# Optimization experiments

Hardware: AMD Instinct MI355X
Metric: run time of the kernel (lower is better)

Reference implementation:

```python
import jax, jax.numpy as jnp
import numpy as np

N, E, IN_DIM, H, HEADS, L, NCLS, NTYPES, NGRAPH = 50000, 800000, 128, 128, 4, 3, 10, 8, 64
C = H // HEADS

def setup_inputs() -> dict:
    key = jax.random.key(0)
    ks = jax.random.split(key, 24)
    inp = {
        'x': jax.random.normal(ks[0], (N, IN_DIM), jnp.float32),
        'edge_index': jax.random.randint(ks[1], (2, E), 0, N, jnp.int64),
        'node_types': jax.random.randint(ks[2], (N,), 0, NTYPES, jnp.int64),
        'batch': jnp.sort(jax.random.randint(ks[3], (N,), 0, NGRAPH, jnp.int64)),
        'W_node': jax.random.normal(ks[4], (IN_DIM, H), jnp.float32) / np.sqrt(IN_DIM),
        'b_node': jnp.zeros((H,), jnp.float32),
        'type_emb': jax.random.normal(ks[5], (NTYPES, H), jnp.float32) * 0.02,
        'W_gat': jax.random.normal(ks[6], (L, H, H), jnp.float32) / np.sqrt(H),
        'a_src': jax.random.normal(ks[7], (L, HEADS, C), jnp.float32) / np.sqrt(C),
        'a_dst': jax.random.normal(ks[8], (L, HEADS, C), jnp.float32) / np.sqrt(C),
        'b_gat': jnp.zeros((L, H), jnp.float32),
        'ln_g': jnp.ones((L, H), jnp.float32),
        'ln_b': jnp.zeros((L, H), jnp.float32),
        'W1': jax.random.normal(ks[9], (H, 2 * H), jnp.float32) / np.sqrt(H),
        'b1': jnp.zeros((2 * H,), jnp.float32),
        'W2': jax.random.normal(ks[10], (2 * H, H), jnp.float32) / np.sqrt(2 * H),
        'b2': jnp.zeros((H,), jnp.float32),
        'W3': jax.random.normal(ks[11], (H, NCLS), jnp.float32) / np.sqrt(H),
        'b3': jnp.zeros((NCLS,), jnp.float32),
    }
    return inp


def _gat_layer(h, src, dst, W, asrc, adst, b):
    # h: [N,H] -> xh: [N,heads,C]
    xh = (h @ W).reshape(N, HEADS, C)
    s_src = jnp.sum(xh * asrc, axis=-1)  # [N,heads]
    s_dst = jnp.sum(xh * adst, axis=-1)
    e = jax.nn.leaky_relu(s_src[src] + s_dst[dst], 0.2)  # [E',heads]
    m = jax.ops.segment_max(e, dst, num_segments=N)      # segment softmax over dst
    ee = jnp.exp(e - m[dst])
    z = jax.ops.segment_sum(ee, dst, num_segments=N)
    alpha = ee / (z[dst] + 1e-16)
    msg = xh[src] * alpha[:, :, None]                    # [E',heads,C]
    out = jax.ops.segment_sum(msg, dst, num_segments=N)
    return out.reshape(N, H) + b


def _layernorm(x, g, b, eps=1e-5):
    mu = jnp.mean(x, -1, keepdims=True)
    var = jnp.mean((x - mu) ** 2, -1, keepdims=True)
    return (x - mu) * jax.lax.rsqrt(var + eps) * g + b


def reference(x, edge_index, node_types, batch, W_node, b_node, type_emb,
              W_gat, a_src, a_dst, b_gat, ln_g, ln_b, W1, b1, W2, b2, W3, b3):
    # PyG GATConv adds self-loops by default
    loops = jnp.arange(N, dtype=edge_index.dtype)
    src = jnp.concatenate([edge_index[0], loops])
    dst = jnp.concatenate([edge_index[1], loops])

    h = x @ W_node + b_node + type_emb[node_types]
    for l in range(L):
        h_prev = h
        h = _gat_layer(h, src, dst, W_gat[l], a_src[l], a_dst[l], b_gat[l])
        h = _layernorm(h, ln_g[l], ln_b[l])
        h = jax.nn.relu(h + h_prev)

    # global_mean_pool over batch (the global-attention h_graph is dead code: overwritten)
    sums = jax.ops.segment_sum(h, batch, num_segments=NGRAPH)
    cnt = jax.ops.segment_sum(jnp.ones((N,), h.dtype), batch, num_segments=NGRAPH)
    hg = sums / jnp.maximum(cnt, 1.0)[:, None]

    z = jax.nn.relu(hg @ W1 + b1)
    z = jax.nn.relu(z @ W2 + b2)
    return z @ W3 + b3
```

## Files before the change

### kernel.cpp

```cpp
#include <hip/hip_runtime.h>
#include <hip/hip_bf16.h>

#define NN 50000
#define EE 800000
#define IN_DIM 128
#define HH 128
#define HEADS 4
#define CC 32
#define LL 3
#define NCLS 10
#define NGRAPH 64
#define SNB ((NN + 1023) / 1024)

using short8 = __attribute__((ext_vector_type(8))) short;
using f32x4 = __attribute__((ext_vector_type(4))) float;

__device__ inline float lrelu(float x) { return fmaxf(x, 0.2f * x); }
__device__ inline float fexp(float x) { return __expf(x); }

__device__ inline float bf2f(ushort u) {
    union { uint32_t i; float f; } c;
    c.i = ((uint32_t)u) << 16;
    return c.f;
}
__device__ inline ushort f2bf(float f) {
    union { float f; uint32_t i; } c;
    c.f = f;
    uint32_t x = c.i;
    uint32_t r = (x + 0x7fffu + ((x >> 16) & 1u)) >> 16;
    return (ushort)r;
}

__device__ inline float wred_sum(float v) {
#pragma unroll
    for (int m = 32; m >= 1; m >>= 1) v += __shfl_xor(v, m, 64);
    return v;
}

__device__ inline float pick4(int h, float a, float b, float c, float d) {
    float ab = (h & 1) ? b : a;
    float cd = (h & 1) ? d : c;
    return (h & 2) ? cd : ab;
}

__global__ __launch_bounds__(256) void convert_x(const float* __restrict__ x,
                                                 ushort* __restrict__ xb) {
    int u = blockIdx.x * 256 + threadIdx.x;
    const float4* x4 = (const float4*)x;
    float4 f0 = x4[u * 2];
    float4 f1 = x4[u * 2 + 1];
    short8 o;
    o[0] = (short)f2bf(f0.x); o[1] = (short)f2bf(f0.y);
    o[2] = (short)f2bf(f0.z); o[3] = (short)f2bf(f0.w);
    o[4] = (short)f2bf(f1.x); o[5] = (short)f2bf(f1.y);
    o[6] = (short)f2bf(f1.z); o[7] = (short)f2bf(f1.w);
    ((short8*)xb)[u] = o;
}

__global__ __launch_bounds__(256) void prep_weights(const float* __restrict__ W_node,
                                                    const float* __restrict__ W_gat,
                                                    ushort* __restrict__ WT) {
    int b = blockIdx.x;
    const float* W = (b == 0) ? W_node : (W_gat + (size_t)(b - 1) * 16384);
    ushort* D = WT + (size_t)b * 16384;
    int t = threadIdx.x;
    int n = t >> 1;
    int k0 = (t & 1) * 64;
    for (int kk = 0; kk < 64; kk++) {
        int k = k0 + kk;
        float v = W[k * 128 + n];
        int u = (k >> 3) ^ (n & 7);
        D[n * 128 + u * 8 + (k & 7)] = f2bf(v);
    }
}

template <int MODE>
__global__ __launch_bounds__(256) void gemm_mfma(
    const ushort* __restrict__ Abf, const ushort* __restrict__ WT,
    ushort* __restrict__ out_bf,
    const float* __restrict__ bias, const int* __restrict__ ntypes,
    const float* __restrict__ temb, int nrows) {
    __shared__ ushort wlds[16384];
    int tid = threadIdx.x;
    int lane = tid & 63;
    int wid = tid >> 6;

    {
        const short8* src = (const short8*)WT;
        short8* dst = (short8*)wlds;
#pragma unroll
        for (int i = 0; i < 8; i++) dst[i * 256 + tid] = src[i * 256 + tid];
    }

    int rbase = blockIdx.x * 64 + wid * 16;
    int arow = rbase + (lane & 15);
    if (arow >= nrows) arow = nrows - 1;
    const short8* arow_p = (const short8*)(Abf + (size_t)arow * 128);
    short8 afr[4];
#pragma unroll
    for (int ks = 0; ks < 4; ks++) afr[ks] = arow_p[ks * 4 + (lane >> 4)];

    __syncthreads();

    f32x4 acc[8];
#pragma unroll
    for (int i = 0; i < 8; i++) acc[i] = (f32x4){0.f, 0.f, 0.f, 0.f};

    int cgrp = lane & 15;
    int kgrp = lane >> 4;
#pragma unroll
    for (int ks = 0; ks < 4; ks++) {
        short8 a = afr[ks];
#pragma unroll
        for (int nt = 0; nt < 8; nt++) {
            int n = nt * 16 + cgrp;
            int u = (ks * 4 + kgrp) ^ (n & 7);
            short8 b = *(const short8*)&wlds[n * 128 + u * 8];
            acc[nt] = __builtin_amdgcn_mfma_f32_16x16x32_bf16(a, b, acc[nt], 0, 0, 0);
        }
    }

    int nts[4];
    if (MODE == 1) {
#pragma unroll
        for (int r = 0; r < 4; r++) {
            int row = rbase + kgrp * 4 + r;
            nts[r] = (row < nrows) ? ntypes[row] : 0;
        }
    }
#pragma unroll
    for (int nt = 0; nt < 8; nt++) {
        int colc = nt * 16 + cgrp;
#pragma unroll
        for (int r = 0; r < 4; r++) {
            int row = rbase + kgrp * 4 + r;
            if (row < nrows) {
                float v = acc[nt][r];
                if (MODE == 1) v += bias[colc] + temb[nts[r] * 128 + colc];
                out_bf[(size_t)row * 128 + colc] = f2bf(v);
            }
        }
    }
}

__global__ __launch_bounds__(256) void attn_scores(
    const ushort* __restrict__ xh, const float* __restrict__ asrc,
    const float* __restrict__ adst, float* __restrict__ s_src,
    float* __restrict__ s_dst, int n) {
    int tid = threadIdx.x;
    int node = blockIdx.x * 16 + (tid >> 4);
    int g = tid & 15;
    if (node >= n) return;
    short8 xv = *(const short8*)(xh + (size_t)node * 128 + g * 8);
    const float4* as4 = (const float4*)(asrc + g * 8);
    const float4* ad4 = (const float4*)(adst + g * 8);
    float4 a0 = as4[0], a1 = as4[1];
    float4 d0 = ad4[0], d1 = ad4[1];
    float xf[8];
#pragma unroll
    for (int k = 0; k < 8; k++) xf[k] = bf2f((ushort)xv[k]);
    float ps = xf[0] * a0.x + xf[1] * a0.y + xf[2] * a0.z + xf[3] * a0.w +
               xf[4] * a1.x + xf[5] * a1.y + xf[6] * a1.z + xf[7] * a1.w;
    float pd = xf[0] * d0.x + xf[1] * d0.y + xf[2] * d0.z + xf[3] * d0.w +
               xf[4] * d1.x + xf[5] * d1.y + xf[6] * d1.z + xf[7] * d1.w;
    ps += __shfl_xor(ps, 1, 64); ps += __shfl_xor(ps, 2, 64);
    pd += __shfl_xor(pd, 1, 64); pd += __shfl_xor(pd, 2, 64);
    if ((g & 3) == 0) {
        s_src[node * 4 + (g >> 2)] = ps;
        s_dst[node * 4 + (g >> 2)] = pd;
    }
}

__global__ void count_slot(const int* __restrict__ dst, int* __restrict__ deg,
                           int* __restrict__ slot, int ne) {
    int i = blockIdx.x * blockDim.x + threadIdx.x;
    if (i < ne) slot[i] = atomicAdd(&deg[dst[i]], 1);
}

__global__ __launch_bounds__(1024) void scan_local(const int* __restrict__ cnt,
                                                   int* __restrict__ rp,
                                                   int* __restrict__ btot, int n) {
    __shared__ int lds[1024];
    int t = threadIdx.x;
    int i = blockIdx.x * 1024 + t;
    int v = (i < n) ? cnt[i] : 0;
    lds[t] = v;
    __syncthreads();
    for (int off = 1; off < 1024; off <<= 1) {
        int u = (t >= off) ? lds[t - off] : 0;
        __syncthreads();
        lds[t] += u;
        __syncthreads();
    }
    if (i < n) rp[i] = lds[t] - v;
    if (t == 1023) btot[blockIdx.x] = lds[1023];
}

__global__ __launch_bounds__(64) void scan_btot(int* __restrict__ btot) {
    int t = threadIdx.x;
    int v = (t < SNB) ? btot[t] : 0;
#pragma unroll
    for (int off = 1; off < 64; off <<= 1) {
        int u = __shfl_up(v, off, 64);
        if (t >= off) v += u;
    }
    if (t < SNB) btot[t] = v;
}

__global__ __launch_bounds__(1024) void scan_add(int* __restrict__ rp,
                                                 const int* __restrict__ btot, int n) {
    int b = blockIdx.x;
    int i = b * 1024 + threadIdx.x;
    int add = (b == 0) ? 0 : btot[b - 1];
    if (i < n) rp[i] += add;
    if (i == 0) rp[n] = EE;
}

__global__ void fill_pass(const int* __restrict__ ei, const int* __restrict__ row_ptr,
                          const int* __restrict__ slot, int* __restrict__ col, int ne) {
    int i = blockIdx.x * blockDim.x + threadIdx.x;
    if (i < ne) {
        int d = ei[ne + i];
        col[row_ptr[d] + slot[i]] = ei[i];
    }
}

__global__ __launch_bounds__(256) void gat_aggregate(
    const ushort* __restrict__ xh, const float* __restrict__ ssrc,
    const float* __restrict__ sdst, const int* __restrict__ row_ptr,
    const int* __restrict__ col, const float* __restrict__ bg,
    const float* __restrict__ lng, const float* __restrict__ lnb,
    ushort* __restrict__ h, int n) {
    int wid = threadIdx.x >> 6;
    int lane = threadIdx.x & 63;
    int node = blockIdx.x * 4 + wid;
    if (node >= n) return;

    int base = row_ptr[node];
    int deg = row_ptr[node + 1] - base;

    float4 sd = ((const float4*)sdst)[node];
    float4 ssf = ((const float4*)ssrc)[node];

    int eg = lane >> 4;
    int g = lane & 15;
    int head = g >> 2;
    float sdH = pick4(head, sd.x, sd.y, sd.z, sd.w);
    float esH = lrelu(pick4(head, ssf.x, ssf.y, ssf.z, ssf.w) + sdH);

    float acc[8];
#pragma unroll
    for (int k = 0; k < 8; k++) acc[k] = 0.f;
    float z = 0.f;

    if (eg == 0) {
        float w = fexp(esH);
        z = w;
        short8 xv = *(const short8*)(xh + (size_t)node * 128 + g * 8);
#pragma unroll
        for (int k = 0; k < 8; k++) acc[k] += w * bf2f((ushort)xv[k]);
    }

    int nit = (deg + 3) >> 2;
#pragma unroll 2
    for (int t = 0; t < nit; t++) {
        int j = t * 4 + eg;
        if (j < deg) {
            int s = col[base + j];
            float4 ss = ((const float4*)ssrc)[s];
            float sH = pick4(head, ss.x, ss.y, ss.z, ss.w);
            float w = fexp(lrelu(sH + sdH));
            z += w;
            short8 xv = *(const short8*)(xh + (size_t)s * 128 + g * 8);
#pragma unroll
            for (int k = 0; k < 8; k++) acc[k] += w * bf2f((ushort)xv[k]);
        }
    }
#pragma unroll
    for (int k = 0; k < 8; k++) {
        acc[k] += __shfl_xor(acc[k], 16, 64);
        acc[k] += __shfl_xor(acc[k], 32, 64);
    }
    z += __shfl_xor(z, 16, 64);
    z += __shfl_xor(z, 32, 64);
    float iz = 1.f / (z + 1e-16f);

    const float4* bg4 = (const float4*)(bg + g * 8);
    float4 b0 = bg4[0], b1 = bg4[1];
    float o[8];
    o[0] = acc[0] * iz + b0.x; o[1] = acc[1] * iz + b0.y;
    o[2] = acc[2] * iz + b0.z; o[3] = acc[3] * iz + b0.w;
    o[4] = acc[4] * iz + b1.x; o[5] = acc[5] * iz + b1.y;
    o[6] = acc[6] * iz + b1.z; o[7] = acc[7] * iz + b1.w;

    float ls = 0.f;
#pragma unroll
    for (int k = 0; k < 8; k++) ls += o[k];
    float mu = wred_sum(ls) * (1.f / 512.f);
    float vs = 0.f;
#pragma unroll
    for (int k = 0; k < 8; k++) {
        o[k] -= mu;
        vs += o[k] * o[k];
    }
    float var = wred_sum(vs) * (1.f / 512.f);
    float rs = rsqrtf(var + 1e-5f);

    if (eg == 0) {
        const float4* lg4 = (const float4*)(lng + g * 8);
        const float4* lb4 = (const float4*)(lnb + g * 8);
        float4 g0 = lg4[0], g1 = lg4[1];
        float4 q0 = lb4[0], q1 = lb4[1];
        ushort* hr = h + (size_t)node * 128 + g * 8;
        short8 prev = *(const short8*)hr;
        float y[8];
        y[0] = fmaxf(o[0] * rs * g0.x + q0.x + bf2f((ushort)prev[0]), 0.f);
        y[1] = fmaxf(o[1] * rs * g0.y + q0.y + bf2f((ushort)prev[1]), 0.f);
        y[2] = fmaxf(o[2] * rs * g0.z + q0.z + bf2f((ushort)prev[2]), 0.f);
        y[3] = fmaxf(o[3] * rs * g0.w + q0.w + bf2f((ushort)prev[3]), 0.f);
        y[4] = fmaxf(o[4] * rs * g1.x + q1.x + bf2f((ushort)prev[4]), 0.f);
        y[5] = fmaxf(o[5] * rs * g1.y + q1.y + bf2f((ushort)prev[5]), 0.f);
        y[6] = fmaxf(o[6] * rs * g1.z + q1.z + bf2f((ushort)prev[6]), 0.f);
        y[7] = fmaxf(o[7] * rs * g1.w + q1.w + bf2f((ushort)prev[7]), 0.f);
        short8 ob;
#pragma unroll
        for (int k = 0; k < 8; k++) ob[k] = (short)f2bf(y[k]);
        *(short8*)hr = ob;
    }
}

__global__ __launch_bounds__(256) void pool_kernel(const ushort* __restrict__ h,
                                                   const int* __restrict__ batch,
                                                   float* __restrict__ sums,
                                                   int* __restrict__ cnts, int n) {
    int c = threadIdx.x & 127;
    int half = threadIdx.x >> 7;
    int n0 = blockIdx.x * 64;
    float acc = 0.f;
    int cur = -1;
    for (int idx = half; idx < 64; idx += 2) {
        int node = n0 + idx;
        if (node >= n) break;
        int g = batch[node];
        if (g != cur) {
            if (cur >= 0) atomicAdd(&sums[cur * 128 + c], acc);
            cur = g;
            acc = 0.f;
        }
        acc += bf2f(h[(size_t)node * 128 + c]);
    }
    if (cur >= 0) atomicAdd(&sums[cur * 128 + c], acc);

    if (c == 0) {
        int cnt = 0, curg = -1;
        for (int idx = half; idx < 64; idx += 2) {
            int node = n0 + idx;
            if (node >= n) break;
            int g = batch[node];
            if (g != curg) {
                if (curg >= 0) atomicAdd(&cnts[curg], cnt);
                curg = g;
                cnt = 0;
            }
            cnt++;
        }
        if (curg >= 0) atomicAdd(&cnts[curg], cnt);
    }
}

__global__ __launch_bounds__(256) void head_kernel(
    const float* __restrict__ sums, const int* __restrict__ cnts,
    const float* __restrict__ W1, const float* __restrict__ b1,
    const float* __restrict__ W2, const float* __restrict__ b2,
    const float* __restrict__ W3, const float* __restrict__ b3,
    float* __restrict__ out) {
    __shared__ float hg[128], z1[256], z2[128];
    int g = blockIdx.x;
    int t = threadIdx.x;
    if (t < 128) hg[t] = sums[g * 128 + t] / fmaxf((float)cnts[g], 1.f);
    __syncthreads();
    {
        float acc = b1[t];
        for (int k = 0; k < 128; k++) acc += hg[k] * W1[k * 256 + t];
        z1[t] = fmaxf(acc, 0.f);
    }
    __syncthreads();
    if (t < 128) {
        float acc = b2[t];
        for (int k = 0; k < 256; k++) acc += z1[k] * W2[k * 128 + t];
        z2[t] = fmaxf(acc, 0.f);
    }
    __syncthreads();
    if (t < NCLS) {
        float acc = b3[t];
        for (int k = 0; k < 128; k++) acc += z2[k] * W3[k * NCLS + t];
        out[g * NCLS + t] = acc;
    }
}

extern "C" void kernel_launch(void* const* d_in, const int* in_sizes, int n_in,
                              void* d_out, int out_size, void* d_ws, size_t ws_size,
                              hipStream_t stream) {
    const float* x = (const float*)d_in[0];
    const int* ei = (const int*)d_in[1];
    const int* ntypes = (const int*)d_in[2];
    const int* batch = (const int*)d_in[3];
    const float* W_node = (const float*)d_in[4];
    const float* b_node = (const float*)d_in[5];
    const float* temb = (const float*)d_in[6];
    const float* W_gat = (const float*)d_in[7];
    const float* a_src = (const float*)d_in[8];
    const float* a_dst = (const float*)d_in[9];
    const float* b_gat = (const float*)d_in[10];
    const float* ln_g = (const float*)d_in[11];
    const float* ln_b = (const float*)d_in[12];
    const float* W1 = (const float*)d_in[13];
    const float* b1 = (const float*)d_in[14];
    const float* W2 = (const float*)d_in[15];
    const float* b2 = (const float*)d_in[16];
    const float* W3 = (const float*)d_in[17];
    const float* b3 = (const float*)d_in[18];
    float* out = (float*)d_out;

    char* ws = (char*)d_ws;
    size_t off = 0;
    auto alloc = [&](size_t bytes) {
        void* p = ws + off;
        off += (bytes + 255) & ~(size_t)255;
        return p;
    };
    ushort* hb = (ushort*)alloc((size_t)NN * 128 * 2);
    ushort* xhb = (ushort*)alloc((size_t)NN * 128 * 2);
    ushort* WT = (ushort*)alloc((size_t)4 * 16384 * 2);
    float* ssrc = (float*)alloc((size_t)NN * 4 * 4);
    float* sdst = (float*)alloc((size_t)NN * 4 * 4);
    int* rowp = (int*)alloc((size_t)(NN + 1) * 4);
    int* fillc = (int*)alloc((size_t)NN * 4);
    int* col = (int*)alloc((size_t)EE * 4);
    int* slot = (int*)alloc((size_t)EE * 4);
    float* psum = (float*)alloc((size_t)NGRAPH * 128 * 4);
    int* pcnt = (int*)alloc((size_t)NGRAPH * 4);
    int* btot = (int*)alloc((size_t)SNB * 4);

    hipError_t e0;
    e0 = hipMemsetAsync(fillc, 0, (size_t)NN * 4, stream); (void)e0;
    e0 = hipMemsetAsync(psum, 0, (size_t)NGRAPH * 128 * 4, stream); (void)e0;
    e0 = hipMemsetAsync(pcnt, 0, (size_t)NGRAPH * 4, stream); (void)e0;

    convert_x<<<3125, 256, 0, stream>>>(x, xhb);
    prep_weights<<<4, 256, 0, stream>>>(W_node, W_gat, WT);

    count_slot<<<(EE + 255) / 256, 256, 0, stream>>>(ei + EE, fillc, slot, EE);
    scan_local<<<SNB, 1024, 0, stream>>>(fillc, rowp, btot, NN);
    scan_btot<<<1, 64, 0, stream>>>(btot);
    scan_add<<<SNB, 1024, 0, stream>>>(rowp, btot, NN);
    fill_pass<<<(EE + 255) / 256, 256, 0, stream>>>(ei, rowp, slot, col, EE);

    int gemm_grid = (NN + 63) / 64;
    gemm_mfma<1><<<gemm_grid, 256, 0, stream>>>(xhb, WT, hb, b_node, ntypes, temb, NN);

    for (int l = 0; l < LL; l++) {
        gemm_mfma<0><<<gemm_grid, 256, 0, stream>>>(hb, WT + (size_t)(l + 1) * 16384, xhb,
                                                    nullptr, nullptr, nullptr, NN);
        attn_scores<<<(NN + 15) / 16, 256, 0, stream>>>(xhb, a_src + l * HEADS * CC,
                                                        a_dst + l * HEADS * CC, ssrc, sdst, NN);
        gat_aggregate<<<(NN + 3) / 4, 256, 0, stream>>>(
            xhb, ssrc, sdst, rowp, col, b_gat + l * 128, ln_g + l * 128, ln_b + l * 128,
            hb, NN);
    }

    pool_kernel<<<(NN + 63) / 64, 256, 0, stream>>>(hb, batch, psum, pcnt, NN);
    head_kernel<<<NGRAPH, 256, 0, stream>>>(psum, pcnt, W1, b1, W2, b2, W3, b3, out);
}
```

Measured before the change: 332.5 us.

## Precompute per-edge attention weights in a separate CSR pass before aggregation

Adds an ew_csr kernel that computes exp(leaky_relu(ssrc[src]+sdst[dst])) for all four heads per edge once and stores them contiguously in CSR order. gat_aggregate then reads the precomputed weight instead of gathering ssrc and doing the exp redundantly in 16 lanes per edge. The inner loop unroll also goes from 2 to 4. The trade-off is an extra kernel launch per layer and a 12.8 MB per-edge buffer that must be written and read back, in exchange for removing a random gather and repeated transcendental work from the aggregation loop.

```diff
diff --git a/kernel.cpp b/kernel.cpp
--- a/kernel.cpp
+++ b/kernel.cpp
@@ -225,12 +225,36 @@
     }
 }
 
+__global__ __launch_bounds__(256) void ew_csr(const int* __restrict__ col,
+                                              const int* __restrict__ row_ptr,
+                                              const float* __restrict__ ssrc,
+                                              const float* __restrict__ sdst,
+                                              float4* __restrict__ ew, int n) {
+    int tid = threadIdx.x;
+    int node = blockIdx.x * 16 + (tid >> 4);
+    int l16 = tid & 15;
+    if (node >= n) return;
+    int base = row_ptr[node];
+    int deg = row_ptr[node + 1] - base;
+    float4 dd = ((const float4*)sdst)[node];
+    for (int j = l16; j < deg; j += 16) {
+        int s = col[base + j];
+        float4 ss = ((const float4*)ssrc)[s];
+        float4 w;
+        w.x = fexp(lrelu(ss.x + dd.x));
+        w.y = fexp(lrelu(ss.y + dd.y));
+        w.z = fexp(lrelu(ss.z + dd.z));
+        w.w = fexp(lrelu(ss.w + dd.w));
+        ew[base + j] = w;
+    }
+}
+
 __global__ __launch_bounds__(256) void gat_aggregate(
     const ushort* __restrict__ xh, const float* __restrict__ ssrc,
-    const float* __restrict__ sdst, const int* __restrict__ row_ptr,
-    const int* __restrict__ col, const float* __restrict__ bg,
-    const float* __restrict__ lng, const float* __restrict__ lnb,
-    ushort* __restrict__ h, int n) {
+    const float* __restrict__ sdst, const float* __restrict__ ew,
+    const int* __restrict__ row_ptr, const int* __restrict__ col,
+    const float* __restrict__ bg, const float* __restrict__ lng,
+    const float* __restrict__ lnb, ushort* __restrict__ h, int n) {
     int wid = threadIdx.x >> 6;
     int lane = threadIdx.x & 63;
     int node = blockIdx.x * 4 + wid;
@@ -262,14 +286,12 @@
     }
 
     int nit = (deg + 3) >> 2;
-#pragma unroll 2
+#pragma unroll 4
     for (int t = 0; t < nit; t++) {
         int j = t * 4 + eg;
         if (j < deg) {
             int s = col[base + j];
-            float4 ss = ((const float4*)ssrc)[s];
-            float sH = pick4(head, ss.x, ss.y, ss.z, ss.w);
-            float w = fexp(lrelu(sH + sdH));
+            float w = ew[(size_t)(base + j) * 4 + head];
             z += w;
             short8 xv = *(const short8*)(xh + (size_t)s * 128 + g * 8);
 #pragma unroll
@@ -438,6 +460,7 @@
     int* fillc = (int*)alloc((size_t)NN * 4);
     int* col = (int*)alloc((size_t)EE * 4);
     int* slot = (int*)alloc((size_t)EE * 4);
+    float* ew = (float*)alloc((size_t)EE * 16);
     float* psum = (float*)alloc((size_t)NGRAPH * 128 * 4);
     int* pcnt = (int*)alloc((size_t)NGRAPH * 4);
     int* btot = (int*)alloc((size_t)SNB * 4);
@@ -464,8 +487,9 @@
                                                     nullptr, nullptr, nullptr, NN);
         attn_scores<<<(NN + 15) / 16, 256, 0, stream>>>(xhb, a_src + l * HEADS * CC,
                                                         a_dst + l * HEADS * CC, ssrc, sdst, NN);
+        ew_csr<<<(NN + 15) / 16, 256, 0, stream>>>(col, rowp, ssrc, sdst, (float4*)ew, NN);
         gat_aggregate<<<(NN + 3) / 4, 256, 0, stream>>>(
-            xhb, ssrc, sdst, rowp, col, b_gat + l * 128, ln_g + l * 128, ln_b + l * 128,
+            xhb, ssrc, sdst, ew, rowp, col, b_gat + l * 128, ln_g + l * 128, ln_b + l * 128,
             hb, NN);
     }
 
```

Result: slower. 351.5 us (+5.7%).
